# Optimization experiments

Measured on AMD Instinct MI355X. Metric: run time of the kernel, lower is better.

Reference implementation:

```python
import jax, jax.numpy as jnp
import numpy as np

N_NODES = 100000
N_EDGES = 3200000
IN_FEATS = 512
HIDDEN = 256
N_CLASSES = 64
NITER = 10
HALT_BIAS_INIT = 3.0


def setup_inputs() -> dict:
    key = jax.random.key(0)
    ks = jax.random.split(key, 8)
    x = jax.random.normal(ks[0], (N_NODES, IN_FEATS), dtype=jnp.float32)
    edge_index = jax.random.randint(ks[1], (2, N_EDGES), 0, N_NODES, dtype=jnp.int64)
    # Linear layers: layers[0]: in->hidden, layers[1]: hidden->classes, halt: classes->1
    W0 = jax.random.normal(ks[2], (IN_FEATS, HIDDEN), dtype=jnp.float32) / np.sqrt(IN_FEATS)
    b0 = jnp.zeros((HIDDEN,), dtype=jnp.float32)
    W1 = jax.random.normal(ks[3], (HIDDEN, N_CLASSES), dtype=jnp.float32) / np.sqrt(HIDDEN)
    b1 = jnp.zeros((N_CLASSES,), dtype=jnp.float32)
    Wh = jax.random.normal(ks[4], (N_CLASSES, 1), dtype=jnp.float32) / np.sqrt(N_CLASSES)
    bh = jnp.full((1,), HALT_BIAS_INIT, dtype=jnp.float32)
    return {"x": x, "edge_index": edge_index, "edge_dropout": 0,
            "W0": W0, "b0": b0, "W1": W1, "b1": b1, "Wh": Wh, "bh": bh}


def reference(x, edge_index, edge_dropout, W0, b0, W1, b1, Wh, bh):
    N = x.shape[0]
    # MLP encoder (eval mode: dropout is identity)
    h = jax.nn.relu(x @ W0 + b0)
    h = h @ W1 + b1                                   # [N, C]

    # gcn_norm with self-loops (edge_dropout=0 in eval => identical every iter)
    loops = jnp.arange(N, dtype=edge_index.dtype)
    row = jnp.concatenate([edge_index[0], loops])     # source
    col = jnp.concatenate([edge_index[1], loops])     # target (aggregation index)
    deg = jax.ops.segment_sum(jnp.ones_like(col, dtype=h.dtype), col, num_segments=N)
    dinv = jnp.where(deg > 0, deg ** -0.5, 0.0)
    norm = dinv[row] * dinv[col]                      # [E+N]

    def step(ph, _):
        msg = norm[:, None] * ph[row]                 # gather + scale, [E+N, C]
        ph2 = jax.ops.segment_sum(msg, col, num_segments=N)  # scatter_add
        logit = jnp.clip(ph2 @ Wh + bh, -10.0, 10.0)  # [N, 1]
        return ph2, (ph2, logit)

    _, (props, logits) = jax.lax.scan(step, h, None, length=NITER)
    outputs = jnp.concatenate([h[None], props], axis=0)       # [niter+1, N, C]
    halting_logits = jnp.transpose(logits[:, :, 0])           # [N, niter]

    lam = jax.nn.sigmoid(halting_logits)
    remain = jnp.cumprod(1.0 - lam, axis=1)                   # inclusive
    remain_excl = jnp.concatenate([jnp.ones((N, 1), lam.dtype), remain[:, :-1]], axis=1)
    p = lam * remain_excl
    p = p.at[:, -1].add(remain[:, -1])                        # leftover mass to last step
    return outputs, p, halting_logits
```

## Files before the change

### kernel.cpp

```cpp
#include <hip/hip_runtime.h>
#include <hip/hip_bf16.h>

#define N_NODES  100000
#define N_EDGES  3200000
#define IN_FEATS 512
#define HIDDEN   256
#define N_CLASSES 64
#define NITER    10

#define SCAN_NB  49

#define OUT_P_OFF  ((size_t)(NITER + 1) * N_NODES * N_CLASSES)
#define OUT_HL_OFF (OUT_P_OFF + (size_t)N_NODES * NITER)

#define WS_META_INTS (4 * N_NODES + 128)
#define WS_CSR_OFF   ((size_t)WS_META_INTS * 4)
#define WS_W0F_OFF   (WS_CSR_OFF + (size_t)2 * N_EDGES * 4)
#define WS_W1F_OFF   (WS_W0F_OFF + 262144)
#define WS_SH0_OFF   (WS_W1F_OFF + 32768)
#define WS_SH1_OFF   (WS_SH0_OFF + (size_t)N_NODES * 64 * 2)
#define WS_NEED_W    (WS_SH0_OFF)
#define WS_NEED_BF   (WS_SH1_OFF + (size_t)N_NODES * 64 * 2)

typedef _Float16 f16x8 __attribute__((ext_vector_type(8)));
typedef _Float16 f16x4 __attribute__((ext_vector_type(4)));
typedef float    f32x4 __attribute__((ext_vector_type(4)));

__device__ __forceinline__ float bflo(unsigned v) { return __uint_as_float(v << 16); }
__device__ __forceinline__ float bfhi(unsigned v) { return __uint_as_float(v & 0xffff0000u); }
__device__ __forceinline__ unsigned short f2bf(float f) {
    unsigned u = __float_as_uint(f);
    return (unsigned short)((u + 0x7fffu + ((u >> 16) & 1u)) >> 16);
}

__global__ void k_detect(const int* ei, int* flag) {
    if (threadIdx.x == 0 && blockIdx.x == 0) {
        int is64 = 1;
        for (int k = 0; k < 128; ++k) {
            if (ei[2 * k + 1] != 0) { is64 = 0; break; }
        }
        *flag = is64;
    }
}

__device__ __forceinline__ int edge_row(const void* ei, int is64, int e) {
    return is64 ? (int)((const long long*)ei)[e] : ((const int*)ei)[e];
}
__device__ __forceinline__ int edge_col(const void* ei, int is64, int e) {
    return is64 ? (int)((const long long*)ei)[(size_t)N_EDGES + e]
                : ((const int*)ei)[(size_t)N_EDGES + e];
}

__global__ void k_count(const void* ei, const int* flag, int* cnt) {
    int e = blockIdx.x * 256 + threadIdx.x;
    if (e >= N_EDGES) return;
    int is64 = *flag;
    atomicAdd(&cnt[edge_col(ei, is64, e)], 1);
}

__global__ __launch_bounds__(256) void k_scan1(const int* cnt, int* part) {
    __shared__ int sd[256];
    int b = blockIdx.x, t = threadIdx.x;
    int s = 0;
    for (int j = t; j < 2048; j += 256) {
        int idx = b * 2048 + j;
        if (idx < N_NODES) s += cnt[idx];
    }
    sd[t] = s;
    __syncthreads();
    for (int o = 128; o > 0; o >>= 1) {
        if (t < o) sd[t] += sd[t + o];
        __syncthreads();
    }
    if (t == 0) part[b] = sd[0];
}

__global__ __launch_bounds__(256) void k_scan2(int* part, int* offs) {
    __shared__ int sd[256];
    int t = threadIdx.x;
    sd[t] = (t < SCAN_NB) ? part[t] : 0;
    __syncthreads();
    for (int o = 1; o < 256; o <<= 1) {
        int add = (t >= o) ? sd[t - o] : 0;
        __syncthreads();
        sd[t] += add;
        __syncthreads();
    }
    if (t < SCAN_NB) part[t] = (t == 0) ? 0 : sd[t - 1];
    if (t == 0) offs[N_NODES] = N_EDGES;
}

__global__ __launch_bounds__(256) void k_scan3(const int* cnt, const int* part, int* offs) {
    __shared__ int sd[256];
    int b = blockIdx.x, t = threadIdx.x;
    int base = b * 2048 + t * 8;
    int local[8];
    int s = 0;
#pragma unroll
    for (int j = 0; j < 8; ++j) {
        int idx = base + j;
        int v = (idx < N_NODES) ? cnt[idx] : 0;
        local[j] = s;
        s += v;
    }
    sd[t] = s;
    __syncthreads();
    for (int o = 1; o < 256; o <<= 1) {
        int add = (t >= o) ? sd[t - o] : 0;
        __syncthreads();
        sd[t] += add;
        __syncthreads();
    }
    int tbase = part[b] + ((t == 0) ? 0 : sd[t - 1]);
#pragma unroll
    for (int j = 0; j < 8; ++j) {
        int idx = base + j;
        if (idx < N_NODES) offs[idx] = tbase + local[j];
    }
}

__global__ void k_dinv(const int* cnt, float* dinv) {
    int i = blockIdx.x * 256 + threadIdx.x;
    if (i >= N_NODES) return;
    dinv[i] = rsqrtf((float)(cnt[i] + 1));
}

#define FILL_GRID 3200
__global__ __launch_bounds__(256) void k_fill_part(const void* ei, const int* flag,
        const float* dinv, const int* offs, int* cursor, int2* csr) {
    const int g = blockIdx.x & 7;
    const int bi = blockIdx.x >> 3;
    const int lo = g * (N_NODES / 8);
    const int hi = lo + (N_NODES / 8);
    const int is64 = *flag;
    const int stride = (FILL_GRID >> 3) * 256;
    for (int e = bi * 256 + threadIdx.x; e < N_EDGES; e += stride) {
        int c = edge_col(ei, is64, e);
        if (c >= lo && c < hi) {
            int r = edge_row(ei, is64, e);
            int pos = offs[c] + atomicAdd(&cursor[c], 1);
            csr[pos] = make_int2(r, __float_as_int(dinv[r] * dinv[c]));
        }
    }
}

__global__ void k_prep_w(const float* __restrict__ W0, const float* __restrict__ W1,
                         _Float16* __restrict__ W0f, _Float16* __restrict__ W1f) {
    int id = blockIdx.x * 256 + threadIdx.x;
    if (id < 16384) {
        int l = id & 63, c = (id >> 6) & 15, kkg = id >> 10;
        int n = c * 16 + (l & 15);
        int kb = kkg * 32 + ((l >> 4) * 8);
        f16x8 v;
#pragma unroll
        for (int j = 0; j < 8; ++j) v[j] = (_Float16)W0[(size_t)(kb + j) * HIDDEN + n];
        *(f16x8*)&W0f[(size_t)id * 8] = v;
    } else if (id < 16384 + 2048) {
        int id2 = id - 16384;
        int l = id2 & 63, c = (id2 >> 6) & 3, kkg = id2 >> 8;
        int n = c * 16 + (l & 15);
        int kb = kkg * 32 + ((l >> 4) * 8);
        f16x8 v;
#pragma unroll
        for (int j = 0; j < 8; ++j) v[j] = (_Float16)W1[(size_t)(kb + j) * N_CLASSES + n];
        *(f16x8*)&W1f[(size_t)id2 * 8] = v;
    }
}

#define EBM 64
#define XS_STRIDE 72
#define H1_STRIDE 264
#define XS0   0
#define XS1   9216
#define WST0  18432
#define WST1  34816
#define W2ST0 34816
#define W2ST1 38912
__global__ __launch_bounds__(256) void k_encoder_mfma(
        const float* __restrict__ x, const _Float16* __restrict__ W0f,
        const float* __restrict__ b0, const _Float16* __restrict__ W1f,
        const float* __restrict__ b1, float* __restrict__ out,
        unsigned short* __restrict__ shadow, int write_shadow) {
    __shared__ char smem[51200];
    const int t = threadIdx.x;
    const int w = t >> 6, l = t & 63;
    const int g = l >> 4, r15 = l & 15;
    const int row0 = blockIdx.x * EBM;
    const int c4 = t & 15;
    const int srow0 = t >> 4;

    f32x4 acc[16];
#pragma unroll
    for (int c = 0; c < 16; ++c) acc[c] = (f32x4){0.f, 0.f, 0.f, 0.f};

    float4 xld[4];
    f16x8 wld[4];
#pragma unroll
    for (int q = 0; q < 4; ++q) {
        int grow = row0 + q * 16 + srow0;
        if (grow >= N_NODES) grow = N_NODES - 1;
        xld[q] = *(const float4*)&x[(size_t)grow * IN_FEATS + c4 * 4];
    }
#pragma unroll
    for (int q = 0; q < 4; ++q) wld[q] = *(const f16x8*)&W0f[(size_t)(q * 256 + t) * 8];
#pragma unroll
    for (int q = 0; q < 4; ++q) {
        f16x4 hv = {(_Float16)xld[q].x, (_Float16)xld[q].y, (_Float16)xld[q].z, (_Float16)xld[q].w};
        *(f16x4*)(smem + XS0 + ((q * 16 + srow0) * XS_STRIDE + c4 * 4) * 2) = hv;
    }
#pragma unroll
    for (int q = 0; q < 4; ++q)
        *(f16x8*)(smem + WST0 + (q * 256 + t) * 16) = wld[q];
    __syncthreads();

    for (int kkg = 0; kkg < 16; ++kkg) {
        const int kc = kkg >> 1, kk = kkg & 1;
        if (kkg < 15) {
#pragma unroll
            for (int q = 0; q < 4; ++q)
                wld[q] = *(const f16x8*)&W0f[(size_t)((kkg + 1) * 1024 + q * 256 + t) * 8];
        }
        if (kk == 0 && kc < 7) {
#pragma unroll
            for (int q = 0; q < 4; ++q) {
                int grow = row0 + q * 16 + srow0;
                if (grow >= N_NODES) grow = N_NODES - 1;
                xld[q] = *(const float4*)&x[(size_t)grow * IN_FEATS + (kc + 1) * 64 + c4 * 4];
            }
        }
        const char* xbase = smem + ((kc & 1) ? XS1 : XS0);
        const char* wbase = smem + ((kkg & 1) ? WST1 : WST0);
        f16x8 af = *(const f16x8*)(xbase + ((w * 16 + r15) * XS_STRIDE + kk * 32 + g * 8) * 2);
#pragma unroll
        for (int c = 0; c < 16; ++c) {
            f16x8 bf = *(const f16x8*)(wbase + ((c << 6) | l) * 16);
            acc[c] = __builtin_amdgcn_mfma_f32_16x16x32_f16(af, bf, acc[c], 0, 0, 0);
        }
        if (kkg < 15) {
            char* wdst = smem + ((kkg & 1) ? WST0 : WST1);
#pragma unroll
            for (int q = 0; q < 4; ++q)
                *(f16x8*)(wdst + (q * 256 + t) * 16) = wld[q];
        }
        if (kk == 1 && kc < 7) {
            char* xdst = smem + ((kc & 1) ? XS0 : XS1);
#pragma unroll
            for (int q = 0; q < 4; ++q) {
                f16x4 hv = {(_Float16)xld[q].x, (_Float16)xld[q].y, (_Float16)xld[q].z, (_Float16)xld[q].w};
                *(f16x4*)(xdst + ((q * 16 + srow0) * XS_STRIDE + c4 * 4) * 2) = hv;
            }
        }
        __syncthreads();
    }

    f16x8 w2ld = *(const f16x8*)&W1f[(size_t)t * 8];
#pragma unroll
    for (int c = 0; c < 16; ++c) {
        float bb = b0[c * 16 + r15];
#pragma unroll
        for (int i = 0; i < 4; ++i) {
            int row = w * 16 + g * 4 + i;
            *(_Float16*)(smem + (row * H1_STRIDE + c * 16 + r15) * 2) =
                (_Float16)fmaxf(acc[c][i] + bb, 0.f);
        }
    }
    *(f16x8*)(smem + W2ST0 + t * 16) = w2ld;
    __syncthreads();

    f32x4 acc2[4];
#pragma unroll
    for (int c = 0; c < 4; ++c) acc2[c] = (f32x4){0.f, 0.f, 0.f, 0.f};
    for (int kkg = 0; kkg < 8; ++kkg) {
        if (kkg < 7) w2ld = *(const f16x8*)&W1f[(size_t)((kkg + 1) * 256 + t) * 8];
        const char* wbase = smem + ((kkg & 1) ? W2ST1 : W2ST0);
        f16x8 af = *(const f16x8*)(smem + ((w * 16 + r15) * H1_STRIDE + kkg * 32 + g * 8) * 2);
#pragma unroll
        for (int c = 0; c < 4; ++c) {
            f16x8 bf = *(const f16x8*)(wbase + ((c << 6) | l) * 16);
            acc2[c] = __builtin_amdgcn_mfma_f32_16x16x32_f16(af, bf, acc2[c], 0, 0, 0);
        }
        if (kkg < 7)
            *(f16x8*)(smem + ((kkg & 1) ? W2ST0 : W2ST1) + t * 16) = w2ld;
        __syncthreads();
    }
#pragma unroll
    for (int c = 0; c < 4; ++c) {
        float bb = b1[c * 16 + r15];
#pragma unroll
        for (int i = 0; i < 4; ++i) {
            int row = row0 + w * 16 + g * 4 + i;
            if (row < N_NODES) {
                float v = acc2[c][i] + bb;
                int col = c * 16 + r15;
                out[(size_t)row * 64 + col] = v;
                if (write_shadow) shadow[(size_t)row * 64 + col] = f2bf(v);
            }
        }
    }
}

__global__ __launch_bounds__(256) void k_encoder(const float* __restrict__ x,
        const float* __restrict__ W0, const float* __restrict__ b0,
        const float* __restrict__ W1, const float* __restrict__ b1,
        float* __restrict__ out) {
    __shared__ float xsh[32][128];
    __shared__ float h1s[32][HIDDEN + 1];
    const int t = threadIdx.x;
    const int rg = t >> 6;
    const int cg = t & 63;
    const size_t row0 = (size_t)blockIdx.x * 32;
    float acc[8][4];
#pragma unroll
    for (int i = 0; i < 8; ++i)
        acc[i][0] = acc[i][1] = acc[i][2] = acc[i][3] = 0.f;
    for (int kc = 0; kc < 4; ++kc) {
        __syncthreads();
#pragma unroll
        for (int q = 0; q < 4; ++q) {
            int idx = t + q * 256;
            int r = idx >> 5, pos = idx & 31;
            *(float4*)&xsh[r][pos * 4] =
                *(const float4*)&x[(row0 + r) * IN_FEATS + kc * 128 + pos * 4];
        }
        __syncthreads();
        for (int kk = 0; kk < 128; kk += 4) {
            float4 xv[8];
#pragma unroll
            for (int i = 0; i < 8; ++i) xv[i] = *(const float4*)&xsh[rg * 8 + i][kk];
#pragma unroll
            for (int j = 0; j < 4; ++j) {
                float4 wv = *(const float4*)&W0[(size_t)(kc * 128 + kk + j) * HIDDEN + cg * 4];
#pragma unroll
                for (int i = 0; i < 8; ++i) {
                    float xj = (&xv[i].x)[j];
                    acc[i][0] = fmaf(xj, wv.x, acc[i][0]);
                    acc[i][1] = fmaf(xj, wv.y, acc[i][1]);
                    acc[i][2] = fmaf(xj, wv.z, acc[i][2]);
                    acc[i][3] = fmaf(xj, wv.w, acc[i][3]);
                }
            }
        }
    }
    float4 bb = *(const float4*)&b0[cg * 4];
#pragma unroll
    for (int i = 0; i < 8; ++i) {
        int r = rg * 8 + i;
        h1s[r][cg * 4 + 0] = fmaxf(acc[i][0] + bb.x, 0.f);
        h1s[r][cg * 4 + 1] = fmaxf(acc[i][1] + bb.y, 0.f);
        h1s[r][cg * 4 + 2] = fmaxf(acc[i][2] + bb.z, 0.f);
        h1s[r][cg * 4 + 3] = fmaxf(acc[i][3] + bb.w, 0.f);
    }
    __syncthreads();
    float a2[8];
#pragma unroll
    for (int i = 0; i < 8; ++i) a2[i] = 0.f;
    for (int k = 0; k < HIDDEN; ++k) {
        float wv = W1[(size_t)k * N_CLASSES + cg];
#pragma unroll
        for (int i = 0; i < 8; ++i) a2[i] = fmaf(h1s[rg * 8 + i][k], wv, a2[i]);
    }
    float bv = b1[cg];
#pragma unroll
    for (int i = 0; i < 8; ++i)
        out[(row0 + rg * 8 + i) * N_CLASSES + cg] = a2[i] + bv;
}

__global__ __launch_bounds__(256) void k_prop_bf(
        const unsigned short* __restrict__ pin_bf, float* __restrict__ pout,
        unsigned short* __restrict__ pout_bf, const int* __restrict__ offs,
        const int2* __restrict__ csr, const float* __restrict__ dinv,
        const float* __restrict__ Wh, const float* __restrict__ bh,
        float* __restrict__ hl, int t) {
    int node = (blockIdx.x * 256 + threadIdx.x) >> 5;
    if (node >= N_NODES) return;
    int hlane = threadIdx.x & 31;
    int base = threadIdx.x & 32;
    float di = dinv[node];
    unsigned vs = *(const unsigned*)&pin_bf[(size_t)node * 64 + hlane * 2];
    float a0 = di * di * bflo(vs), a1 = di * di * bfhi(vs);
    float c0 = 0.f, c1 = 0.f;
    int e0 = offs[node], e1 = offs[node + 1];
    for (int eb = e0; eb < e1; eb += 32) {
        int n = e1 - eb; if (n > 32) n = 32;
        int idx = eb + hlane;
        int2 ew = csr[idx < e1 ? idx : e1 - 1];
        int j = 0;
        for (; j + 16 <= n; j += 16) {
            unsigned v[16]; float w[16];
#pragma unroll
            for (int q = 0; q < 16; ++q) {
                int s = __shfl(ew.x, base + j + q, 64);
                w[q] = __int_as_float(__shfl(ew.y, base + j + q, 64));
                v[q] = *(const unsigned*)&pin_bf[(size_t)s * 64 + hlane * 2];
            }
#pragma unroll
            for (int q = 0; q < 16; ++q) {
                if (q & 1) { c0 = fmaf(w[q], bflo(v[q]), c0); c1 = fmaf(w[q], bfhi(v[q]), c1); }
                else       { a0 = fmaf(w[q], bflo(v[q]), a0); a1 = fmaf(w[q], bfhi(v[q]), a1); }
            }
        }
        for (; j + 8 <= n; j += 8) {
            unsigned v[8]; float w[8];
#pragma unroll
            for (int q = 0; q < 8; ++q) {
                int s = __shfl(ew.x, base + j + q, 64);
                w[q] = __int_as_float(__shfl(ew.y, base + j + q, 64));
                v[q] = *(const unsigned*)&pin_bf[(size_t)s * 64 + hlane * 2];
            }
#pragma unroll
            for (int q = 0; q < 8; ++q) {
                if (q & 1) { c0 = fmaf(w[q], bflo(v[q]), c0); c1 = fmaf(w[q], bfhi(v[q]), c1); }
                else       { a0 = fmaf(w[q], bflo(v[q]), a0); a1 = fmaf(w[q], bfhi(v[q]), a1); }
            }
        }
        for (; j < n; ++j) {
            int s = __shfl(ew.x, base + j, 64);
            float w = __int_as_float(__shfl(ew.y, base + j, 64));
            unsigned v = *(const unsigned*)&pin_bf[(size_t)s * 64 + hlane * 2];
            a0 = fmaf(w, bflo(v), a0);
            a1 = fmaf(w, bfhi(v), a1);
        }
    }
    float fa = a0 + c0, fb = a1 + c1;
    *(float2*)&pout[(size_t)node * 64 + hlane * 2] = make_float2(fa, fb);
    *(unsigned*)&pout_bf[(size_t)node * 64 + hlane * 2] =
        (unsigned)f2bf(fa) | ((unsigned)f2bf(fb) << 16);
    float2 wh = *(const float2*)&Wh[hlane * 2];
    float s = fa * wh.x + fb * wh.y;
#pragma unroll
    for (int o = 16; o > 0; o >>= 1) s += __shfl_xor(s, o, 64);
    if (hlane == 0) {
        float lg = s + bh[0];
        lg = fminf(10.0f, fmaxf(-10.0f, lg));
        hl[(size_t)node * NITER + t] = lg;
    }
}

__global__ __launch_bounds__(256) void k_prop(const float* __restrict__ pin,
        float* __restrict__ pout, const int* __restrict__ offs,
        const int2* __restrict__ csr, const float* __restrict__ dinv,
        const float* __restrict__ Wh, const float* __restrict__ bh,
        float* __restrict__ hl, int t) {
    int wid = (blockIdx.x * blockDim.x + threadIdx.x) >> 6;
    int lane = threadIdx.x & 63;
    if (wid >= N_NODES) return;
    float di = dinv[wid];
    float a[4];
    a[0] = di * di * pin[(size_t)wid * 64 + lane];
    a[1] = a[2] = a[3] = 0.f;
    int e0 = offs[wid], e1 = offs[wid + 1];
    for (int eb = e0; eb < e1; eb += 64) {
        int n = e1 - eb; if (n > 64) n = 64;
        int idx = eb + lane;
        int2 ew = csr[idx < e1 ? idx : e1 - 1];
        int j = 0;
        for (; j + 8 <= n; j += 8) {
            float v[8], w[8];
#pragma unroll
            for (int q = 0; q < 8; ++q) {
                int s = __shfl(ew.x, j + q, 64);
                w[q] = __int_as_float(__shfl(ew.y, j + q, 64));
                v[q] = pin[(size_t)s * 64 + lane];
            }
#pragma unroll
            for (int q = 0; q < 8; ++q) a[q & 3] = fmaf(w[q], v[q], a[q & 3]);
        }
        for (; j < n; ++j) {
            int s = __shfl(ew.x, j, 64);
            float w = __int_as_float(__shfl(ew.y, j, 64));
            a[0] = fmaf(w, pin[(size_t)s * 64 + lane], a[0]);
        }
    }
    float acc = (a[0] + a[1]) + (a[2] + a[3]);
    pout[(size_t)wid * 64 + lane] = acc;
    float s = acc * Wh[lane];
#pragma unroll
    for (int o = 32; o > 0; o >>= 1) s += __shfl_xor(s, o, 64);
    if (lane == 0) {
        float lg = s + bh[0];
        lg = fminf(10.0f, fmaxf(-10.0f, lg));
        hl[(size_t)wid * NITER + t] = lg;
    }
}

__global__ void k_p(const float* __restrict__ hl, float* __restrict__ p) {
    int i = blockIdx.x * 256 + threadIdx.x;
    if (i >= N_NODES) return;
    float remain = 1.0f;
    float pv[NITER];
#pragma unroll
    for (int t = 0; t < NITER; ++t) {
        float lg = hl[(size_t)i * NITER + t];
        float lam = 1.0f / (1.0f + expf(-lg));
        pv[t] = lam * remain;
        remain *= (1.0f - lam);
    }
    pv[NITER - 1] += remain;
#pragma unroll
    for (int t = 0; t < NITER; ++t) p[(size_t)i * NITER + t] = pv[t];
}

extern "C" void kernel_launch(void* const* d_in, const int* in_sizes, int n_in,
                              void* d_out, int out_size, void* d_ws, size_t ws_size,
                              hipStream_t stream) {
    const float* x  = (const float*)d_in[0];
    const void*  ei = d_in[1];
    const float* W0 = (const float*)d_in[3];
    const float* b0 = (const float*)d_in[4];
    const float* W1 = (const float*)d_in[5];
    const float* b1 = (const float*)d_in[6];
    const float* Wh = (const float*)d_in[7];
    const float* bh = (const float*)d_in[8];
    float* out = (float*)d_out;

    int* ws_i   = (int*)d_ws;
    int* cnt    = ws_i;
    int* offs   = ws_i + N_NODES;
    int* cursor = ws_i + 2 * N_NODES + 2;
    int* part   = ws_i + 3 * N_NODES + 2;
    int* flag   = ws_i + 3 * N_NODES + 66;
    float* dinv = (float*)(ws_i + 3 * N_NODES + 128);
    int2* csr   = (int2*)((char*)d_ws + WS_CSR_OFF);
    _Float16* W0f = (_Float16*)((char*)d_ws + WS_W0F_OFF);
    _Float16* W1f = (_Float16*)((char*)d_ws + WS_W1F_OFF);
    unsigned short* sh0 = (unsigned short*)((char*)d_ws + WS_SH0_OFF);
    unsigned short* sh1 = (unsigned short*)((char*)d_ws + WS_SH1_OFF);

    const int use_w  = ws_size >= WS_NEED_W;
    const int use_bf = ws_size >= WS_NEED_BF;

    hipMemsetAsync(d_ws, 0, (size_t)(3 * N_NODES + 128) * 4, stream);
    k_detect<<<1, 64, 0, stream>>>((const int*)ei, flag);
    k_count<<<(N_EDGES + 255) / 256, 256, 0, stream>>>(ei, flag, cnt);
    k_scan1<<<SCAN_NB, 256, 0, stream>>>(cnt, part);
    k_scan2<<<1, 256, 0, stream>>>(part, offs);
    k_scan3<<<SCAN_NB, 256, 0, stream>>>(cnt, part, offs);
    k_dinv<<<(N_NODES + 255) / 256, 256, 0, stream>>>(cnt, dinv);
    k_fill_part<<<FILL_GRID, 256, 0, stream>>>(ei, flag, dinv, offs, cursor, csr);

    if (use_w) {
        k_prep_w<<<72, 256, 0, stream>>>(W0, W1, W0f, W1f);
        k_encoder_mfma<<<(N_NODES + EBM - 1) / EBM, 256, 0, stream>>>(
            x, W0f, b0, W1f, b1, out, sh0, use_bf);
    } else {
        k_encoder<<<N_NODES / 32, 256, 0, stream>>>(x, W0, b0, W1, b1, out);
    }

    float* hl = out + OUT_HL_OFF;
    if (use_bf) {
        for (int it = 0; it < NITER; ++it) {
            const unsigned short* pin_bf = (it & 1) ? sh1 : sh0;
            unsigned short* pout_bf      = (it & 1) ? sh0 : sh1;
            float* pout = out + (size_t)(it + 1) * N_NODES * N_CLASSES;
            k_prop_bf<<<((size_t)N_NODES * 32 + 255) / 256, 256, 0, stream>>>(
                pin_bf, pout, pout_bf, offs, csr, dinv, Wh, bh, hl, it);
        }
    } else {
        for (int it = 0; it < NITER; ++it) {
            const float* pin = out + (size_t)it * N_NODES * N_CLASSES;
            float* pout      = out + (size_t)(it + 1) * N_NODES * N_CLASSES;
            k_prop<<<((size_t)N_NODES * 64 + 255) / 256, 256, 0, stream>>>(
                pin, pout, offs, csr, dinv, Wh, bh, hl, it);
        }
    }
    k_p<<<(N_NODES + 255) / 256, 256, 0, stream>>>(hl, out + OUT_P_OFF);
}
```

Baseline: 1.065 ms.

## Build CSR through a two-pass bucket binning instead of eightfold edge rescans

During counting, the edges are also histogrammed into 128-node buckets, each split into 8 subgroups by chunk, and those counts are scanned into bin offsets. A binning kernel then scatters (row, col) pairs into the buckets. A per-bucket fill kernel builds the CSR using shared-memory cursors instead of global atomics. This replaces the old partitioned fill, where each of 8 node groups re-read the whole edge list. The cost is an extra 25.6 MB of workspace plus an extra write and read of the binned edges.

```diff
diff --git a/kernel.cpp b/kernel.cpp
--- a/kernel.cpp
+++ b/kernel.cpp
@@ -9,6 +9,10 @@
 #define NITER    10
 
 #define SCAN_NB  49
+#define NBKT     782
+#define NSUB     (NBKT * 8)
+#define A1_GRID  2048
+#define NCHUNK   (N_EDGES / 256)
 
 #define OUT_P_OFF  ((size_t)(NITER + 1) * N_NODES * N_CLASSES)
 #define OUT_HL_OFF (OUT_P_OFF + (size_t)N_NODES * NITER)
@@ -19,8 +23,10 @@
 #define WS_W1F_OFF   (WS_W0F_OFF + 262144)
 #define WS_SH0_OFF   (WS_W1F_OFF + 32768)
 #define WS_SH1_OFF   (WS_SH0_OFF + (size_t)N_NODES * 64 * 2)
+#define WS_BIN_OFF   (WS_SH1_OFF + (size_t)N_NODES * 64 * 2)
 #define WS_NEED_W    (WS_SH0_OFF)
-#define WS_NEED_BF   (WS_SH1_OFF + (size_t)N_NODES * 64 * 2)
+#define WS_NEED_BF   (WS_BIN_OFF)
+#define WS_NEED_BIN  (WS_BIN_OFF + (size_t)N_EDGES * 8)
 
 typedef _Float16 f16x8 __attribute__((ext_vector_type(8)));
 typedef _Float16 f16x4 __attribute__((ext_vector_type(4)));
@@ -51,11 +57,22 @@
                 : ((const int*)ei)[(size_t)N_EDGES + e];
 }
 
-__global__ void k_count(const void* ei, const int* flag, int* cnt) {
-    int e = blockIdx.x * 256 + threadIdx.x;
-    if (e >= N_EDGES) return;
+__global__ __launch_bounds__(256) void k_count_hist(const void* ei, const int* flag,
+        int* cnt, int* bhist) {
+    __shared__ int lh[NSUB];
+    for (int i = threadIdx.x; i < NSUB; i += 256) lh[i] = 0;
+    __syncthreads();
     int is64 = *flag;
-    atomicAdd(&cnt[edge_col(ei, is64, e)], 1);
+    for (int e = blockIdx.x * 256 + threadIdx.x; e < N_EDGES; e += 1024 * 256) {
+        int c = edge_col(ei, is64, e);
+        atomicAdd(&cnt[c], 1);
+        atomicAdd(&lh[(c >> 7) * 8 + ((e >> 8) & 7)], 1);
+    }
+    __syncthreads();
+    for (int i = threadIdx.x; i < NSUB; i += 256) {
+        int v = lh[i];
+        if (v) atomicAdd(&bhist[i], v);
+    }
 }
 
 __global__ __launch_bounds__(256) void k_scan1(const int* cnt, int* part) {
@@ -119,10 +136,71 @@
     }
 }
 
+__global__ __launch_bounds__(256) void k_scan6k(const int* bhist, int* binoffs) {
+    __shared__ int sd[256];
+    int t = threadIdx.x;
+    int base = t * 25;
+    int loc[25];
+    int s = 0;
+#pragma unroll
+    for (int j = 0; j < 25; ++j) {
+        int idx = base + j;
+        int v = (idx < NSUB) ? bhist[idx] : 0;
+        loc[j] = s;
+        s += v;
+    }
+    sd[t] = s;
+    __syncthreads();
+    for (int o = 1; o < 256; o <<= 1) {
+        int add = (t >= o) ? sd[t - o] : 0;
+        __syncthreads();
+        sd[t] += add;
+        __syncthreads();
+    }
+    int tb = (t == 0) ? 0 : sd[t - 1];
+#pragma unroll
+    for (int j = 0; j < 25; ++j) {
+        int idx = base + j;
+        if (idx < NSUB) binoffs[idx] = tb + loc[j];
+    }
+    if (t == 255) binoffs[NSUB] = N_EDGES;
+}
+
 __global__ void k_dinv(const int* cnt, float* dinv) {
     int i = blockIdx.x * 256 + threadIdx.x;
     if (i >= N_NODES) return;
     dinv[i] = rsqrtf((float)(cnt[i] + 1));
+}
+
+__global__ __launch_bounds__(256) void k_bin(const void* ei, const int* flag,
+        const int* __restrict__ binoffs, int* __restrict__ bincur,
+        int2* __restrict__ bin) {
+    int is64 = *flag;
+    int B = blockIdx.x, g = B & 7;
+    for (int ci = B; ci < NCHUNK; ci += A1_GRID) {
+        int e = ci * 256 + threadIdx.x;
+        int c = edge_col(ei, is64, e);
+        int r = edge_row(ei, is64, e);
+        int idx = (c >> 7) * 8 + g;
+        int pos = binoffs[idx] + atomicAdd(&bincur[idx], 1);
+        bin[pos] = make_int2(r, c);
+    }
+}
+
+__global__ __launch_bounds__(256) void k_fill_b(const int2* __restrict__ bin,
+        const int* __restrict__ binoffs, const int* __restrict__ offs,
+        const float* __restrict__ dinv, int2* __restrict__ csr) {
+    __shared__ int lcur[128];
+    int b = blockIdx.x;
+    int lo = b << 7;
+    if (threadIdx.x < 128) lcur[threadIdx.x] = 0;
+    __syncthreads();
+    int start = binoffs[b * 8], end = binoffs[(b + 1) * 8];
+    for (int i = start + threadIdx.x; i < end; i += 256) {
+        int2 rc = bin[i];
+        int pos = offs[rc.y] + atomicAdd(&lcur[rc.y - lo], 1);
+        csr[pos] = make_int2(rc.x, __float_as_int(dinv[rc.x] * dinv[rc.y]));
+    }
 }
 
 #define FILL_GRID 3200
@@ -517,6 +595,9 @@
     int* cnt    = ws_i;
     int* offs   = ws_i + N_NODES;
     int* cursor = ws_i + 2 * N_NODES + 2;
+    int* bhist   = cursor;
+    int* binoffs = cursor + 8192;
+    int* bincur  = cursor + 16384;
     int* part   = ws_i + 3 * N_NODES + 2;
     int* flag   = ws_i + 3 * N_NODES + 66;
     float* dinv = (float*)(ws_i + 3 * N_NODES + 128);
@@ -525,18 +606,26 @@
     _Float16* W1f = (_Float16*)((char*)d_ws + WS_W1F_OFF);
     unsigned short* sh0 = (unsigned short*)((char*)d_ws + WS_SH0_OFF);
     unsigned short* sh1 = (unsigned short*)((char*)d_ws + WS_SH1_OFF);
-
-    const int use_w  = ws_size >= WS_NEED_W;
-    const int use_bf = ws_size >= WS_NEED_BF;
+    int2* bin = (int2*)((char*)d_ws + WS_BIN_OFF);
+
+    const int use_w   = ws_size >= WS_NEED_W;
+    const int use_bf  = ws_size >= WS_NEED_BF;
+    const int use_bin = ws_size >= WS_NEED_BIN;
 
     hipMemsetAsync(d_ws, 0, (size_t)(3 * N_NODES + 128) * 4, stream);
     k_detect<<<1, 64, 0, stream>>>((const int*)ei, flag);
-    k_count<<<(N_EDGES + 255) / 256, 256, 0, stream>>>(ei, flag, cnt);
+    k_count_hist<<<1024, 256, 0, stream>>>(ei, flag, cnt, bhist);
     k_scan1<<<SCAN_NB, 256, 0, stream>>>(cnt, part);
     k_scan2<<<1, 256, 0, stream>>>(part, offs);
     k_scan3<<<SCAN_NB, 256, 0, stream>>>(cnt, part, offs);
     k_dinv<<<(N_NODES + 255) / 256, 256, 0, stream>>>(cnt, dinv);
-    k_fill_part<<<FILL_GRID, 256, 0, stream>>>(ei, flag, dinv, offs, cursor, csr);
+    if (use_bin) {
+        k_scan6k<<<1, 256, 0, stream>>>(bhist, binoffs);
+        k_bin<<<A1_GRID, 256, 0, stream>>>(ei, flag, binoffs, bincur, bin);
+        k_fill_b<<<NBKT, 256, 0, stream>>>(bin, binoffs, offs, dinv, csr);
+    } else {
+        k_fill_part<<<FILL_GRID, 256, 0, stream>>>(ei, flag, dinv, offs, bincur + 8192, csr);
+    }
 
     if (use_w) {
         k_prep_w<<<72, 256, 0, stream>>>(W0, W1, W0f, W1f);
```

Result: slower. 1.114 ms (+4.6%).
